# Optimization experiments

Measured on AMD Instinct MI355X. Metric: run time of the kernel, lower is better.

## Reference

```python
import jax, jax.numpy as jnp
import numpy as np

B, L, S = 4, 1024, 1024
D_MODEL, H, DK = 1024, 16, 64  # d_model == H * DK required by the in-place writeback


def setup_inputs() -> dict:
    key = jax.random.key(0)
    ks = jax.random.split(key, 12)
    queries = jax.random.normal(ks[0], (B, L, D_MODEL), dtype=jnp.float32)
    keys = jax.random.normal(ks[1], (B, S, D_MODEL), dtype=jnp.float32)
    values = jax.random.normal(ks[2], (B, S, D_MODEL), dtype=jnp.float32)
    gate_scores = jax.random.uniform(ks[3], (B, H, DK, D_MODEL), dtype=jnp.float32)
    sc = 1.0 / np.sqrt(D_MODEL)
    W_q = jax.random.normal(ks[4], (H * DK, D_MODEL), dtype=jnp.float32) * sc
    b_q = jax.random.normal(ks[5], (H * DK,), dtype=jnp.float32) * 0.01
    W_k = jax.random.normal(ks[6], (H * DK, D_MODEL), dtype=jnp.float32) * sc
    b_k = jax.random.normal(ks[7], (H * DK,), dtype=jnp.float32) * 0.01
    W_v = jax.random.normal(ks[8], (H * DK, D_MODEL), dtype=jnp.float32) * sc
    b_v = jax.random.normal(ks[9], (H * DK,), dtype=jnp.float32) * 0.01
    W_o = jax.random.normal(ks[10], (D_MODEL, H * DK), dtype=jnp.float32) * sc
    b_o = jax.random.normal(ks[11], (D_MODEL,), dtype=jnp.float32) * 0.01
    return {"queries": queries, "keys": keys, "values": values,
            "gate_scores": gate_scores, "W_q": W_q, "b_q": b_q,
            "W_k": W_k, "b_k": b_k, "W_v": W_v, "b_v": b_v,
            "W_o": W_o, "b_o": b_o}


def reference(queries, keys, values, gate_scores, W_q, b_q, W_k, b_k, W_v, b_v, W_o, b_o):
    # Per-sample gated Q/K/V projection: W_x[b] = gate_scores[b] * W_x  (elementwise, [H,DK,Dm])
    # fused as a batched einsum instead of the per-sample Python loop.
    Wq = W_q.reshape(H, DK, D_MODEL)
    Wk = W_k.reshape(H, DK, D_MODEL)
    Wv = W_v.reshape(H, DK, D_MODEL)
    Q = jnp.einsum('blm,bhkm,hkm->blhk', queries, gate_scores, Wq) + b_q.reshape(H, DK)
    K = jnp.einsum('bsm,bhkm,hkm->bshk', keys, gate_scores, Wk) + b_k.reshape(H, DK)
    V = jnp.einsum('bsm,bhkm,hkm->bshk', values, gate_scores, Wv) + b_v.reshape(H, DK)
    # Full scaled dot-product attention (standard inner_attention)
    scale = 1.0 / jnp.sqrt(jnp.asarray(DK, Q.dtype))
    scores = jnp.einsum('blhk,bshk->bhls', Q, K) * scale
    attn = jax.nn.softmax(scores, axis=-1)
    out = jnp.einsum('bhls,bshk->blhk', attn, V).reshape(B, L, H * DK)
    out = out @ W_o.T + b_o
    return out, attn
```

## Files before the change

### kernel.cpp

```cpp
#include <hip/hip_runtime.h>
#include <math.h>

#define BB 4
#define LL 1024
#define SS 1024
#define DM 1024
#define HH 16
#define DKH 64
#define NH 1024
#define QK_ALPHA 0.1803368801f

typedef __attribute__((ext_vector_type(8))) short bf16x8;
typedef __attribute__((ext_vector_type(4))) float f32x4;
typedef unsigned short ushort_t;
typedef unsigned int uint_t;

#define MFMA16(a, b, c) __builtin_amdgcn_mfma_f32_16x16x32_bf16((a), (b), (c), 0, 0, 0)

__device__ __forceinline__ ushort_t f2b(float f) {
    union { float f; uint_t u; } x; x.f = f;
    uint_t r = x.u + 0x7fffu + ((x.u >> 16) & 1u);
    return (ushort_t)(r >> 16);
}

__device__ __forceinline__ float b2f(ushort_t v) {
    union { float f; uint_t u; } x; x.u = ((uint_t)v) << 16;
    return x.f;
}

__device__ __forceinline__ void gload_lds16(const void* g, void* l) {
    __builtin_amdgcn_global_load_lds(
        (const __attribute__((address_space(1))) unsigned int*)g,
        (__attribute__((address_space(3))) unsigned int*)l, 16, 0, 0);
}

__device__ __forceinline__ int xcd_swz(int lin, int nwg) {
    return (lin & 7) * (nwg >> 3) + (lin >> 3);
}

__device__ __forceinline__ void cvt8(const float* src, ushort_t* dst, const float* g2) {
    float4 a  = *(const float4*)(src);
    float4 b4 = *(const float4*)(src + 4);
    if (g2) {
        float4 ga = *(const float4*)(g2);
        float4 gb = *(const float4*)(g2 + 4);
        a.x *= ga.x; a.y *= ga.y; a.z *= ga.z; a.w *= ga.w;
        b4.x *= gb.x; b4.y *= gb.y; b4.z *= gb.z; b4.w *= gb.w;
    }
    uint4 o;
    o.x = f2b(a.x)  | ((uint_t)f2b(a.y)  << 16);
    o.y = f2b(a.z)  | ((uint_t)f2b(a.w)  << 16);
    o.z = f2b(b4.x) | ((uint_t)f2b(b4.y) << 16);
    o.w = f2b(b4.z) | ((uint_t)f2b(b4.w) << 16);
    *(uint4*)dst = o;
}

__global__ __launch_bounds__(256) void prep_kernel(
    const float* __restrict__ q, const float* __restrict__ k, const float* __restrict__ v,
    const float* __restrict__ gate,
    const float* __restrict__ Wq, const float* __restrict__ Wk, const float* __restrict__ Wv,
    const float* __restrict__ Wo,
    ushort_t* __restrict__ Xq, ushort_t* __restrict__ Xk, ushort_t* __restrict__ Xv,
    ushort_t* __restrict__ Gq, ushort_t* __restrict__ Gk, ushort_t* __restrict__ Gv,
    ushort_t* __restrict__ Wo2)
{
    const int XCH = 3 * 524288;
    const int GCH = 524288;
    const int WCH = 131072;
    for (int c = blockIdx.x * 256 + threadIdx.x; c < XCH + GCH + WCH; c += gridDim.x * 256) {
        if (c < XCH) {
            int r = c >> 19;
            int e = (c & 524287) * 8;
            cvt8((r == 0 ? q : r == 1 ? k : v) + e,
                 (r == 0 ? Xq : r == 1 ? Xk : Xv) + e, nullptr);
        } else if (c < XCH + GCH) {
            int e = (c - XCH) * 8;
            int nm = e & 1048575;
            const float* g2 = gate + e;
            cvt8(Wq + nm, Gq + e, g2);
            cvt8(Wk + nm, Gk + e, g2);
            cvt8(Wv + nm, Gv + e, g2);
        } else {
            int e = (c - XCH - GCH) * 8;
            cvt8(Wo + e, Wo2 + e, nullptr);
        }
    }
}

__global__ __launch_bounds__(256) void qkv_gemm(
    const ushort_t* __restrict__ Xq, const ushort_t* __restrict__ Gq, const float* __restrict__ bq,
    const ushort_t* __restrict__ Xk, const ushort_t* __restrict__ Gk, const float* __restrict__ bk,
    const ushort_t* __restrict__ Xv, const ushort_t* __restrict__ Gv, const float* __restrict__ bv,
    ushort_t* __restrict__ Qb, ushort_t* __restrict__ Kb, ushort_t* __restrict__ Vt,
    int mode)
{
    __shared__ ushort_t As[128 * 64];
    __shared__ ushort_t Bs[128 * 64];
    const int p  = xcd_swz(blockIdx.x, gridDim.x);
    const int g2 = p >> 6;
    const int r  = p & 63;
    int b, g;
    if (mode == 0)      { b = g2 / 3;  g = g2 % 3; }
    else if (mode == 1) { b = g2 >> 1; g = g2 & 1; }
    else                { b = g2;      g = 2;      }
    const size_t off = (size_t)b * 1048576;
    const ushort_t *A, *B; const float* bias; ushort_t* C; bool brow;
    if (g == 0)      { A = Xq + off; B = Gq + off; bias = bq; C = Qb + off; brow = false; }
    else if (g == 1) { A = Xk + off; B = Gk + off; bias = bk; C = Kb + off; brow = false; }
    else             { A = Gv + off; B = Xv + off; bias = bv; C = Vt + off; brow = true;  }
    const float oscale = (g == 0) ? QK_ALPHA : 1.0f;

    const int bm = (r >> 3) * 128;
    const int bn = (r & 7) * 128;
    const int tid = threadIdx.x;
    const int lane = tid & 63;
    const int w = tid >> 6;
    const int wr = w >> 1, wc = w & 1;
    const int lr = lane & 15, lk = lane >> 4;

    f32x4 acc[4][4];
    #pragma unroll
    for (int i = 0; i < 4; ++i)
        #pragma unroll
        for (int j = 0; j < 4; ++j)
            acc[i][j] = (f32x4){0.f, 0.f, 0.f, 0.f};

    for (int k0 = 0; k0 < 1024; k0 += 64) {
        #pragma unroll
        for (int pp = 0; pp < 4; ++pp) {
            int f = pp * 256 + tid;
            int row = f >> 3, seg = f & 7;
            int kb2 = (seg * 8) ^ ((row & 7) * 8);
            gload_lds16(A + (size_t)(bm + row) * 1024 + k0 + kb2,
                        (char*)As + ((pp * 256 + (w << 6)) << 4));
            gload_lds16(B + (size_t)(bn + row) * 1024 + k0 + kb2,
                        (char*)Bs + ((pp * 256 + (w << 6)) << 4));
        }
        __syncthreads();
        #pragma unroll
        for (int kk = 0; kk < 2; ++kk) {
            bf16x8 af[4], bfr[4];
            #pragma unroll
            for (int i = 0; i < 4; ++i) {
                int row = wr * 64 + i * 16 + lr;
                af[i] = *(const bf16x8*)&As[row * 64 + ((lk * 8 + kk * 32) ^ ((row & 7) * 8))];
            }
            #pragma unroll
            for (int j = 0; j < 4; ++j) {
                int row = wc * 64 + j * 16 + lr;
                bfr[j] = *(const bf16x8*)&Bs[row * 64 + ((lk * 8 + kk * 32) ^ ((row & 7) * 8))];
            }
            #pragma unroll
            for (int i = 0; i < 4; ++i)
                #pragma unroll
                for (int j = 0; j < 4; ++j)
                    acc[i][j] = MFMA16(af[i], bfr[j], acc[i][j]);
        }
        __syncthreads();
    }

    #pragma unroll
    for (int i = 0; i < 4; ++i)
        #pragma unroll
        for (int j = 0; j < 4; ++j)
            #pragma unroll
            for (int rr = 0; rr < 4; ++rr) {
                int row = bm + wr * 64 + i * 16 + lk * 4 + rr;
                int col = bn + wc * 64 + j * 16 + lr;
                float vv = (acc[i][j][rr] + bias[brow ? row : col]) * oscale;
                C[(size_t)row * 1024 + col] = f2b(vv);
            }
}

__global__ __launch_bounds__(512) void fused_attn_kernel(
    const ushort_t* __restrict__ Q, const ushort_t* __restrict__ Kmat,
    const ushort_t* __restrict__ Vt, float* __restrict__ attn,
    ushort_t* __restrict__ ctx)
{
    __shared__ ushort_t K2[2][64 * 64];
    __shared__ ushort_t V2[2][64 * 64];
    __shared__ ushort_t Ps[8 * 1024];
    const int p  = xcd_swz(blockIdx.x, gridDim.x);
    const int bh = p >> 3;
    const int b  = bh >> 4;
    const int h  = bh & 15;
    const int r0 = (p & 7) * 128;
    const int tid = threadIdx.x, lane = tid & 63, w = tid >> 6;
    const int lr = lane & 15, lk = lane >> 4;

    bf16x8 aq[2];
    {
        const ushort_t* Qrow = Q + ((size_t)b * LL + r0 + w * 16 + lr) * NH + h * DKH;
        aq[0] = *(const bf16x8*)(Qrow + lk * 8);
        aq[1] = *(const bf16x8*)(Qrow + lk * 8 + 32);
    }
    const ushort_t* Kp = Kmat + (size_t)b * SS * NH + h * DKH;
    const ushort_t* Vp = Vt + ((size_t)b * NH + h * DKH) * SS;
    ushort_t* Psw = Ps + w * 1024;

    const int srow = tid >> 3;
    const int sseg = tid & 7;
    const int skb  = (sseg * 8) ^ ((srow & 7) * 8);

#define STAGE_K(t, buf)                                                         \
    gload_lds16(Kp + (size_t)((t) * 64 + srow) * NH + skb,                      \
                (char*)(&K2[buf][0]) + (w << 10))
#define STAGE_V(t, buf)                                                         \
    gload_lds16(Vp + (size_t)srow * SS + (t) * 64 + skb,                        \
                (char*)(&V2[buf][0]) + (w << 10))

    float inv[4] = {0.f, 0.f, 0.f, 0.f};

    STAGE_K(0, 0);
    __syncthreads();
    for (int t = 0; t < 16; ++t) {
        const int cur = t & 1;
        if (t < 15) STAGE_K(t + 1, cur ^ 1);
        f32x4 acc[4];
        #pragma unroll
        for (int j = 0; j < 4; ++j) acc[j] = (f32x4){0.f, 0.f, 0.f, 0.f};
        #pragma unroll
        for (int kk = 0; kk < 2; ++kk)
            #pragma unroll
            for (int j = 0; j < 4; ++j) {
                int row = j * 16 + lr;
                bf16x8 bk2 = *(const bf16x8*)&K2[cur][row * 64 + ((lk * 8 + kk * 32) ^ ((row & 7) * 8))];
                acc[j] = MFMA16(aq[kk], bk2, acc[j]);
            }
        #pragma unroll
        for (int rr = 0; rr < 4; ++rr)
            inv[rr] += __builtin_amdgcn_exp2f(acc[0][rr]) + __builtin_amdgcn_exp2f(acc[1][rr])
                     + __builtin_amdgcn_exp2f(acc[2][rr]) + __builtin_amdgcn_exp2f(acc[3][rr]);
        __syncthreads();
    }
    #pragma unroll
    for (int rr = 0; rr < 4; ++rr) {
        float s = inv[rr];
        s += __shfl_xor(s, 1);
        s += __shfl_xor(s, 2);
        s += __shfl_xor(s, 4);
        s += __shfl_xor(s, 8);
        inv[rr] = 1.0f / s;
    }

    f32x4 occ[4];
    #pragma unroll
    for (int j = 0; j < 4; ++j) occ[j] = (f32x4){0.f, 0.f, 0.f, 0.f};
    float* Ob = attn + (((size_t)b * HH + h) * LL + r0 + w * 16) * SS;
    const int erow = lane >> 3;
    const int eseg = lane & 7;

    STAGE_K(0, 0);
    STAGE_V(0, 0);
    __syncthreads();
    for (int t = 0; t < 16; ++t) {
        const int cur = t & 1;
        if (t < 15) { STAGE_K(t + 1, cur ^ 1); STAGE_V(t + 1, cur ^ 1); }
        f32x4 acc[4];
        #pragma unroll
        for (int j = 0; j < 4; ++j) acc[j] = (f32x4){0.f, 0.f, 0.f, 0.f};
        #pragma unroll
        for (int kk = 0; kk < 2; ++kk)
            #pragma unroll
            for (int j = 0; j < 4; ++j) {
                int row = j * 16 + lr;
                bf16x8 bk2 = *(const bf16x8*)&K2[cur][row * 64 + ((lk * 8 + kk * 32) ^ ((row & 7) * 8))];
                acc[j] = MFMA16(aq[kk], bk2, acc[j]);
            }
        #pragma unroll
        for (int j = 0; j < 4; ++j)
            #pragma unroll
            for (int rr = 0; rr < 4; ++rr) {
                int ql = lk * 4 + rr;
                float pv = __builtin_amdgcn_exp2f(acc[j][rr]) * inv[rr];
                Psw[ql * 64 + ((j * 16 + lr) ^ ((ql & 7) * 8))] = f2b(pv);
            }
        #pragma unroll
        for (int kk = 0; kk < 2; ++kk) {
            bf16x8 pa = *(const bf16x8*)&Psw[lr * 64 + ((kk * 32 + lk * 8) ^ ((lr & 7) * 8))];
            #pragma unroll
            for (int j = 0; j < 4; ++j) {
                int row = j * 16 + lr;
                bf16x8 bv2 = *(const bf16x8*)&V2[cur][row * 64 + ((kk * 32 + lk * 8) ^ ((row & 7) * 8))];
                occ[j] = MFMA16(pa, bv2, occ[j]);
            }
        }
        float* Obt = Ob + t * 64;
        #pragma unroll
        for (int hh = 0; hh < 2; ++hh) {
            int rl = erow + hh * 8;
            bf16x8 p8 = *(const bf16x8*)&Psw[rl * 64 + ((eseg * 8) ^ ((rl & 7) * 8))];
            float4 o0 = make_float4(b2f((ushort_t)p8[0]), b2f((ushort_t)p8[1]),
                                    b2f((ushort_t)p8[2]), b2f((ushort_t)p8[3]));
            float4 o1 = make_float4(b2f((ushort_t)p8[4]), b2f((ushort_t)p8[5]),
                                    b2f((ushort_t)p8[6]), b2f((ushort_t)p8[7]));
            *(float4*)(Obt + (size_t)rl * SS + eseg * 8) = o0;
            *(float4*)(Obt + (size_t)rl * SS + eseg * 8 + 4) = o1;
        }
        __syncthreads();
    }

    #pragma unroll
    for (int j = 0; j < 4; ++j)
        #pragma unroll
        for (int rr = 0; rr < 4; ++rr)
            ctx[((size_t)b * LL + r0 + w * 16 + lk * 4 + rr) * NH + h * DKH + j * 16 + lr]
                = f2b(occ[j][rr]);
#undef STAGE_K
#undef STAGE_V
}

__global__ __launch_bounds__(256) void out_gemm(
    const ushort_t* __restrict__ A, const ushort_t* __restrict__ B,
    const float* __restrict__ bias, float* __restrict__ C)
{
    __shared__ ushort_t As[128 * 64];
    __shared__ ushort_t Bs[64 * 64];
    const int p  = xcd_swz(blockIdx.x, gridDim.x);
    const int bm = (p >> 4) * 128;
    const int bn = (p & 15) * 64;
    const int tid = threadIdx.x;
    const int lane = tid & 63;
    const int w = tid >> 6;
    const int wr = w >> 1, wc = w & 1;
    const int lr = lane & 15, lk = lane >> 4;

    f32x4 acc[4][2];
    #pragma unroll
    for (int i = 0; i < 4; ++i)
        #pragma unroll
        for (int j = 0; j < 2; ++j)
            acc[i][j] = (f32x4){0.f, 0.f, 0.f, 0.f};

    for (int k0 = 0; k0 < 1024; k0 += 64) {
        #pragma unroll
        for (int pp = 0; pp < 4; ++pp) {
            int f = pp * 256 + tid;
            int row = f >> 3, seg = f & 7;
            int kb2 = (seg * 8) ^ ((row & 7) * 8);
            gload_lds16(A + (size_t)(bm + row) * 1024 + k0 + kb2,
                        (char*)As + ((pp * 256 + (w << 6)) << 4));
        }
        #pragma unroll
        for (int pp = 0; pp < 2; ++pp) {
            int f = pp * 256 + tid;
            int row = f >> 3, seg = f & 7;
            int kb2 = (seg * 8) ^ ((row & 7) * 8);
            gload_lds16(B + (size_t)(bn + row) * 1024 + k0 + kb2,
                        (char*)Bs + ((pp * 256 + (w << 6)) << 4));
        }
        __syncthreads();
        #pragma unroll
        for (int kk = 0; kk < 2; ++kk) {
            bf16x8 af[4], bfr[2];
            #pragma unroll
            for (int i = 0; i < 4; ++i) {
                int row = wr * 64 + i * 16 + lr;
                af[i] = *(const bf16x8*)&As[row * 64 + ((lk * 8 + kk * 32) ^ ((row & 7) * 8))];
            }
            #pragma unroll
            for (int j = 0; j < 2; ++j) {
                int row = wc * 32 + j * 16 + lr;
                bfr[j] = *(const bf16x8*)&Bs[row * 64 + ((lk * 8 + kk * 32) ^ ((row & 7) * 8))];
            }
            #pragma unroll
            for (int i = 0; i < 4; ++i)
                #pragma unroll
                for (int j = 0; j < 2; ++j)
                    acc[i][j] = MFMA16(af[i], bfr[j], acc[i][j]);
        }
        __syncthreads();
    }

    #pragma unroll
    for (int i = 0; i < 4; ++i)
        #pragma unroll
        for (int j = 0; j < 2; ++j)
            #pragma unroll
            for (int rr = 0; rr < 4; ++rr) {
                int row = bm + wr * 64 + i * 16 + lk * 4 + rr;
                int col = bn + wc * 32 + j * 16 + lr;
                C[(size_t)row * DM + col] = acc[i][j][rr] + bias[col];
            }
}

extern "C" void kernel_launch(void* const* d_in, const int* in_sizes, int n_in,
                              void* d_out, int out_size, void* d_ws, size_t ws_size,
                              hipStream_t stream)
{
    const float* queries = (const float*)d_in[0];
    const float* keys    = (const float*)d_in[1];
    const float* values  = (const float*)d_in[2];
    const float* gate    = (const float*)d_in[3];
    const float* W_q     = (const float*)d_in[4];
    const float* b_q     = (const float*)d_in[5];
    const float* W_k     = (const float*)d_in[6];
    const float* b_k     = (const float*)d_in[7];
    const float* W_v     = (const float*)d_in[8];
    const float* b_v     = (const float*)d_in[9];
    const float* W_o     = (const float*)d_in[10];
    const float* b_o     = (const float*)d_in[11];

    float* out  = (float*)d_out;
    float* attn = out + (size_t)BB * LL * DM;

    char* ws = (char*)d_ws;
    const size_t U = (size_t)8 << 20;
    ushort_t* Xq = (ushort_t*)(ws);
    ushort_t* Xk = (ushort_t*)(ws + 1 * U);
    ushort_t* Xv = (ushort_t*)(ws + 2 * U);
    ushort_t* Gq = (ushort_t*)(ws + 3 * U);
    ushort_t* Gk = (ushort_t*)(ws + 4 * U);
    ushort_t* Gv = (ushort_t*)(ws + 5 * U);
    ushort_t* Vt = (ushort_t*)(ws + 6 * U);
    const bool big = ws_size >= 9 * U + ((size_t)2 << 20);
    ushort_t *Qb, *Kb, *Wo2;
    if (big) { Qb = (ushort_t*)(ws + 7 * U); Kb = (ushort_t*)(ws + 8 * U); Wo2 = (ushort_t*)(ws + 9 * U); }
    else     { Qb = Xv; Kb = Gv; Wo2 = (ushort_t*)(ws + 7 * U); }
    ushort_t* ctx = Xq;

    dim3 blk(256, 1, 1);
    prep_kernel<<<2048, blk, 0, stream>>>(queries, keys, values, gate,
                                          W_q, W_k, W_v, W_o,
                                          Xq, Xk, Xv, Gq, Gk, Gv, Wo2);
    if (big) {
        qkv_gemm<<<768, blk, 0, stream>>>(Xq, Gq, b_q, Xk, Gk, b_k,
                                          Xv, Gv, b_v, Qb, Kb, Vt, 0);
    } else {
        qkv_gemm<<<256, blk, 0, stream>>>(Xq, Gq, b_q, Xk, Gk, b_k,
                                          Xv, Gv, b_v, Qb, Kb, Vt, 2);
        qkv_gemm<<<512, blk, 0, stream>>>(Xq, Gq, b_q, Xk, Gk, b_k,
                                          Xv, Gv, b_v, Qb, Kb, Vt, 1);
    }
    fused_attn_kernel<<<512, dim3(512, 1, 1), 0, stream>>>(Qb, Kb, Vt, attn, ctx);
    out_gemm<<<512, blk, 0, stream>>>(ctx, Wo2, b_o, out);
}
```

Before: 174.5 us.

## Give each attention wave two 16-row query tiles and halve block size

The fused attention kernel now runs 4 waves (256 threads) per block instead of 8, and each wave handles 32 query rows instead of 16. Every K/V fragment read from LDS feeds two MFMAs, which halves LDS reads per FLOP. Each thread now issues two staging loads for K and V. The cost is more registers per wave and fewer waves per block to hide latency, which may reduce occupancy.

```diff
diff --git a/kernel.cpp b/kernel.cpp
--- a/kernel.cpp
+++ b/kernel.cpp
@@ -172,14 +172,14 @@
             }
 }
 
-__global__ __launch_bounds__(512) void fused_attn_kernel(
+__global__ __launch_bounds__(256) void fused_attn_kernel(
     const ushort_t* __restrict__ Q, const ushort_t* __restrict__ Kmat,
     const ushort_t* __restrict__ Vt, float* __restrict__ attn,
     ushort_t* __restrict__ ctx)
 {
     __shared__ ushort_t K2[2][64 * 64];
     __shared__ ushort_t V2[2][64 * 64];
-    __shared__ ushort_t Ps[8 * 1024];
+    __shared__ ushort_t Ps[4 * 2048];
     const int p  = xcd_swz(blockIdx.x, gridDim.x);
     const int bh = p >> 3;
     const int b  = bh >> 4;
@@ -188,65 +188,84 @@
     const int tid = threadIdx.x, lane = tid & 63, w = tid >> 6;
     const int lr = lane & 15, lk = lane >> 4;
 
-    bf16x8 aq[2];
-    {
-        const ushort_t* Qrow = Q + ((size_t)b * LL + r0 + w * 16 + lr) * NH + h * DKH;
-        aq[0] = *(const bf16x8*)(Qrow + lk * 8);
-        aq[1] = *(const bf16x8*)(Qrow + lk * 8 + 32);
+    bf16x8 aq[2][2];
+    #pragma unroll
+    for (int i = 0; i < 2; ++i) {
+        const ushort_t* Qrow = Q + ((size_t)b * LL + r0 + w * 32 + i * 16 + lr) * NH + h * DKH;
+        aq[i][0] = *(const bf16x8*)(Qrow + lk * 8);
+        aq[i][1] = *(const bf16x8*)(Qrow + lk * 8 + 32);
     }
     const ushort_t* Kp = Kmat + (size_t)b * SS * NH + h * DKH;
     const ushort_t* Vp = Vt + ((size_t)b * NH + h * DKH) * SS;
-    ushort_t* Psw = Ps + w * 1024;
+    ushort_t* Psw = Ps + w * 2048;
 
     const int srow = tid >> 3;
     const int sseg = tid & 7;
     const int skb  = (sseg * 8) ^ ((srow & 7) * 8);
-
-#define STAGE_K(t, buf)                                                         \
-    gload_lds16(Kp + (size_t)((t) * 64 + srow) * NH + skb,                      \
-                (char*)(&K2[buf][0]) + (w << 10))
-#define STAGE_V(t, buf)                                                         \
-    gload_lds16(Vp + (size_t)srow * SS + (t) * 64 + skb,                        \
-                (char*)(&V2[buf][0]) + (w << 10))
-
-    float inv[4] = {0.f, 0.f, 0.f, 0.f};
+    const int skb1 = (sseg * 8) ^ (((srow + 32) & 7) * 8);
+
+#define STAGE_K(t, buf)                                                          \
+    do {                                                                         \
+        gload_lds16(Kp + (size_t)((t) * 64 + srow) * NH + skb,                   \
+                    (char*)(&K2[buf][0]) + ((0 * 256 + (w << 6)) << 4));         \
+        gload_lds16(Kp + (size_t)((t) * 64 + srow + 32) * NH + skb1,             \
+                    (char*)(&K2[buf][0]) + ((1 * 256 + (w << 6)) << 4));         \
+    } while (0)
+#define STAGE_V(t, buf)                                                          \
+    do {                                                                         \
+        gload_lds16(Vp + (size_t)srow * SS + (t) * 64 + skb,                     \
+                    (char*)(&V2[buf][0]) + ((0 * 256 + (w << 6)) << 4));         \
+        gload_lds16(Vp + (size_t)(srow + 32) * SS + (t) * 64 + skb1,             \
+                    (char*)(&V2[buf][0]) + ((1 * 256 + (w << 6)) << 4));         \
+    } while (0)
+
+    float inv[2][4] = {{0.f, 0.f, 0.f, 0.f}, {0.f, 0.f, 0.f, 0.f}};
 
     STAGE_K(0, 0);
     __syncthreads();
     for (int t = 0; t < 16; ++t) {
         const int cur = t & 1;
         if (t < 15) STAGE_K(t + 1, cur ^ 1);
-        f32x4 acc[4];
-        #pragma unroll
-        for (int j = 0; j < 4; ++j) acc[j] = (f32x4){0.f, 0.f, 0.f, 0.f};
+        f32x4 acc[2][4];
+        #pragma unroll
+        for (int i = 0; i < 2; ++i)
+            #pragma unroll
+            for (int j = 0; j < 4; ++j) acc[i][j] = (f32x4){0.f, 0.f, 0.f, 0.f};
         #pragma unroll
         for (int kk = 0; kk < 2; ++kk)
             #pragma unroll
             for (int j = 0; j < 4; ++j) {
                 int row = j * 16 + lr;
                 bf16x8 bk2 = *(const bf16x8*)&K2[cur][row * 64 + ((lk * 8 + kk * 32) ^ ((row & 7) * 8))];
-                acc[j] = MFMA16(aq[kk], bk2, acc[j]);
-            }
-        #pragma unroll
-        for (int rr = 0; rr < 4; ++rr)
-            inv[rr] += __builtin_amdgcn_exp2f(acc[0][rr]) + __builtin_amdgcn_exp2f(acc[1][rr])
-                     + __builtin_amdgcn_exp2f(acc[2][rr]) + __builtin_amdgcn_exp2f(acc[3][rr]);
-        __syncthreads();
-    }
-    #pragma unroll
-    for (int rr = 0; rr < 4; ++rr) {
-        float s = inv[rr];
-        s += __shfl_xor(s, 1);
-        s += __shfl_xor(s, 2);
-        s += __shfl_xor(s, 4);
-        s += __shfl_xor(s, 8);
-        inv[rr] = 1.0f / s;
-    }
-
-    f32x4 occ[4];
-    #pragma unroll
-    for (int j = 0; j < 4; ++j) occ[j] = (f32x4){0.f, 0.f, 0.f, 0.f};
-    float* Ob = attn + (((size_t)b * HH + h) * LL + r0 + w * 16) * SS;
+                acc[0][j] = MFMA16(aq[0][kk], bk2, acc[0][j]);
+                acc[1][j] = MFMA16(aq[1][kk], bk2, acc[1][j]);
+            }
+        #pragma unroll
+        for (int i = 0; i < 2; ++i)
+            #pragma unroll
+            for (int rr = 0; rr < 4; ++rr)
+                inv[i][rr] += __builtin_amdgcn_exp2f(acc[i][0][rr]) + __builtin_amdgcn_exp2f(acc[i][1][rr])
+                            + __builtin_amdgcn_exp2f(acc[i][2][rr]) + __builtin_amdgcn_exp2f(acc[i][3][rr]);
+        __syncthreads();
+    }
+    #pragma unroll
+    for (int i = 0; i < 2; ++i)
+        #pragma unroll
+        for (int rr = 0; rr < 4; ++rr) {
+            float s = inv[i][rr];
+            s += __shfl_xor(s, 1);
+            s += __shfl_xor(s, 2);
+            s += __shfl_xor(s, 4);
+            s += __shfl_xor(s, 8);
+            inv[i][rr] = 1.0f / s;
+        }
+
+    f32x4 occ[2][4];
+    #pragma unroll
+    for (int i = 0; i < 2; ++i)
+        #pragma unroll
+        for (int j = 0; j < 4; ++j) occ[i][j] = (f32x4){0.f, 0.f, 0.f, 0.f};
+    float* Ob = attn + (((size_t)b * HH + h) * LL + r0 + w * 32) * SS;
     const int erow = lane >> 3;
     const int eseg = lane & 7;
 
@@ -256,38 +275,45 @@
     for (int t = 0; t < 16; ++t) {
         const int cur = t & 1;
         if (t < 15) { STAGE_K(t + 1, cur ^ 1); STAGE_V(t + 1, cur ^ 1); }
-        f32x4 acc[4];
-        #pragma unroll
-        for (int j = 0; j < 4; ++j) acc[j] = (f32x4){0.f, 0.f, 0.f, 0.f};
+        f32x4 acc[2][4];
+        #pragma unroll
+        for (int i = 0; i < 2; ++i)
+            #pragma unroll
+            for (int j = 0; j < 4; ++j) acc[i][j] = (f32x4){0.f, 0.f, 0.f, 0.f};
         #pragma unroll
         for (int kk = 0; kk < 2; ++kk)
             #pragma unroll
             for (int j = 0; j < 4; ++j) {
                 int row = j * 16 + lr;
                 bf16x8 bk2 = *(const bf16x8*)&K2[cur][row * 64 + ((lk * 8 + kk * 32) ^ ((row & 7) * 8))];
-                acc[j] = MFMA16(aq[kk], bk2, acc[j]);
-            }
-        #pragma unroll
-        for (int j = 0; j < 4; ++j)
-            #pragma unroll
-            for (int rr = 0; rr < 4; ++rr) {
-                int ql = lk * 4 + rr;
-                float pv = __builtin_amdgcn_exp2f(acc[j][rr]) * inv[rr];
-                Psw[ql * 64 + ((j * 16 + lr) ^ ((ql & 7) * 8))] = f2b(pv);
-            }
+                acc[0][j] = MFMA16(aq[0][kk], bk2, acc[0][j]);
+                acc[1][j] = MFMA16(aq[1][kk], bk2, acc[1][j]);
+            }
+        #pragma unroll
+        for (int i = 0; i < 2; ++i)
+            #pragma unroll
+            for (int j = 0; j < 4; ++j)
+                #pragma unroll
+                for (int rr = 0; rr < 4; ++rr) {
+                    int ql = i * 16 + lk * 4 + rr;
+                    float pv = __builtin_amdgcn_exp2f(acc[i][j][rr]) * inv[i][rr];
+                    Psw[ql * 64 + ((j * 16 + lr) ^ ((ql & 7) * 8))] = f2b(pv);
+                }
         #pragma unroll
         for (int kk = 0; kk < 2; ++kk) {
-            bf16x8 pa = *(const bf16x8*)&Psw[lr * 64 + ((kk * 32 + lk * 8) ^ ((lr & 7) * 8))];
+            bf16x8 pa0 = *(const bf16x8*)&Psw[lr * 64 + ((kk * 32 + lk * 8) ^ ((lr & 7) * 8))];
+            bf16x8 pa1 = *(const bf16x8*)&Psw[(16 + lr) * 64 + ((kk * 32 + lk * 8) ^ ((lr & 7) * 8))];
             #pragma unroll
             for (int j = 0; j < 4; ++j) {
                 int row = j * 16 + lr;
                 bf16x8 bv2 = *(const bf16x8*)&V2[cur][row * 64 + ((kk * 32 + lk * 8) ^ ((row & 7) * 8))];
-                occ[j] = MFMA16(pa, bv2, occ[j]);
+                occ[0][j] = MFMA16(pa0, bv2, occ[0][j]);
+                occ[1][j] = MFMA16(pa1, bv2, occ[1][j]);
             }
         }
         float* Obt = Ob + t * 64;
         #pragma unroll
-        for (int hh = 0; hh < 2; ++hh) {
+        for (int hh = 0; hh < 4; ++hh) {
             int rl = erow + hh * 8;
             bf16x8 p8 = *(const bf16x8*)&Psw[rl * 64 + ((eseg * 8) ^ ((rl & 7) * 8))];
             float4 o0 = make_float4(b2f((ushort_t)p8[0]), b2f((ushort_t)p8[1]),
@@ -301,11 +327,13 @@
     }
 
     #pragma unroll
-    for (int j = 0; j < 4; ++j)
-        #pragma unroll
-        for (int rr = 0; rr < 4; ++rr)
-            ctx[((size_t)b * LL + r0 + w * 16 + lk * 4 + rr) * NH + h * DKH + j * 16 + lr]
-                = f2b(occ[j][rr]);
+    for (int i = 0; i < 2; ++i)
+        #pragma unroll
+        for (int j = 0; j < 4; ++j)
+            #pragma unroll
+            for (int rr = 0; rr < 4; ++rr)
+                ctx[((size_t)b * LL + r0 + w * 32 + i * 16 + lk * 4 + rr) * NH + h * DKH + j * 16 + lr]
+                    = f2b(occ[i][j][rr]);
 #undef STAGE_K
 #undef STAGE_V
 }
@@ -432,6 +460,6 @@
         qkv_gemm<<<512, blk, 0, stream>>>(Xq, Gq, b_q, Xk, Gk, b_k,
                                           Xv, Gv, b_v, Qb, Kb, Vt, 1);
     }
-    fused_attn_kernel<<<512, dim3(512, 1, 1), 0, stream>>>(Qb, Kb, Vt, attn, ctx);
+    fused_attn_kernel<<<512, blk, 0, stream>>>(Qb, Kb, Vt, attn, ctx);
     out_gemm<<<512, blk, 0, stream>>>(ctx, Wo2, b_o, out);
 }
```

New measurement: 182.6 us. +4.7%, slower.
